# Optimization experiments

Measured on AMD Instinct MI355X. Metric: run time of the kernel, lower is better.

The kernel has to match this reference:

```python
import jax, jax.numpy as jnp
import numpy as np

N_BINS = 15


def setup_inputs() -> dict:
    key = jax.random.key(0)
    k1, k2 = jax.random.split(key)
    N, C = 2000000, 64
    probabilities = jax.random.uniform(k1, (N, C), dtype=jnp.float32)
    labels = jax.random.randint(k2, (N,), 0, C, dtype=jnp.int64)
    return {"probabilities": probabilities, "labels": labels}


def reference(probabilities, labels):
    # confidences/predictions over class dim
    confidences = jnp.max(probabilities, axis=1)
    predictions = jnp.argmax(probabilities, axis=1)
    accuracies = (predictions == labels).astype(confidences.dtype)

    boundaries = jnp.linspace(0.0, 1.0, N_BINS + 1)
    # torch loop uses (lower, upper] bins; digitize(right=True) gives index i
    # s.t. boundaries[i-1] < x <= boundaries[i]. conf == 0 falls in no bin.
    bin_idx = jnp.clip(jnp.digitize(confidences, boundaries, right=True) - 1, 0, N_BINS - 1)
    valid = (confidences > 0).astype(confidences.dtype)

    sum_conf = jax.ops.segment_sum(confidences * valid, bin_idx, num_segments=N_BINS)
    sum_acc = jax.ops.segment_sum(accuracies * valid, bin_idx, num_segments=N_BINS)
    count = jax.ops.segment_sum(valid, bin_idx, num_segments=N_BINS)

    n = confidences.shape[0]
    prop_in_bin = count / n
    safe = jnp.maximum(count, 1.0)
    avg_conf = sum_conf / safe
    avg_acc = sum_acc / safe
    per_bin = jnp.where(count > 0, jnp.abs(avg_conf - avg_acc) * prop_in_bin, 0.0)
    ece = jnp.sum(per_bin)
    return ece.reshape(1)
```

## Files before the change

kernel.cpp:

```cpp
#include <hip/hip_runtime.h>
#include <hip/hip_bf16.h>

#define N_BINS 15
#define C_DIM 64


__global__ void ece_main(const float* __restrict__ probs,
                         const int* __restrict__ labels,
                         float* __restrict__ gbins, int N) {
    __shared__ float s_conf[N_BINS];
    __shared__ float s_acc[N_BINS];
    __shared__ float s_cnt[N_BINS];

    const int tid = threadIdx.x;
    if (tid < N_BINS) { s_conf[tid] = 0.f; s_acc[tid] = 0.f; s_cnt[tid] = 0.f; }
    __syncthreads();

    const int lane = tid & 63;
    const int wave = tid >> 6;
    const int sub  = lane >> 4;
    const int l16  = lane & 15;
    const int wavesPerBlock = blockDim.x >> 6;

    long long g      = (long long)blockIdx.x * wavesPerBlock + wave;
    const long long gstride = (long long)gridDim.x * wavesPerBlock;

    for (; g * 4 < (long long)N; g += gstride) {
        const long long row = g * 4 + sub;
        const bool rowvalid = row < (long long)N;

        float conf; int pred;
        if (rowvalid) {
            const float4 v = *(const float4*)(probs + row * C_DIM + l16 * 4);
            float m = v.x; int a = l16 * 4;
            if (v.y > m) { m = v.y; a = l16 * 4 + 1; }
            if (v.z > m) { m = v.z; a = l16 * 4 + 2; }
            if (v.w > m) { m = v.w; a = l16 * 4 + 3; }
            conf = m; pred = a;
        } else {
            conf = -1.f; pred = 0;
        }

        #pragma unroll
        for (int off = 1; off < 16; off <<= 1) {
            float om = __shfl_xor(conf, off, 64);
            int   oa = __shfl_xor(pred, off, 64);
            if (om > conf || (om == conf && oa < pred)) { conf = om; pred = oa; }
        }

        if (l16 == 0 && rowvalid) {
            const int lab = labels[row];
            const float acc = (pred == lab) ? 1.f : 0.f;
            if (conf > 0.f) {
                int bin = (int)ceilf(conf * 15.f) - 1;
                bin = min(max(bin, 0), N_BINS - 1);
                atomicAdd(&s_conf[bin], conf);
                atomicAdd(&s_acc[bin], acc);
                atomicAdd(&s_cnt[bin], 1.f);
            }
        }
    }

    __syncthreads();
    if (tid < N_BINS) {
        atomicAdd(&gbins[tid],              s_conf[tid]);
        atomicAdd(&gbins[N_BINS + tid],     s_acc[tid]);
        atomicAdd(&gbins[2 * N_BINS + tid], s_cnt[tid]);
    }
}

__global__ void ece_final(const float* __restrict__ gbins,
                          float* __restrict__ out, int N) {
    if (threadIdx.x == 0 && blockIdx.x == 0) {
        float ece = 0.f;
        const float invN = 1.f / (float)N;
        for (int b = 0; b < N_BINS; b++) {
            const float sc = gbins[b];
            const float sa = gbins[N_BINS + b];
            const float cn = gbins[2 * N_BINS + b];
            if (cn > 0.f) {
                const float avg_conf = sc / cn;
                const float avg_acc  = sa / cn;
                ece += fabsf(avg_conf - avg_acc) * (cn * invN);
            }
        }
        out[0] = ece;
    }
}

extern "C" void kernel_launch(void* const* d_in, const int* in_sizes, int n_in,
                              void* d_out, int out_size, void* d_ws, size_t ws_size,
                              hipStream_t stream) {
    const float* probs  = (const float*)d_in[0];
    const int*   labels = (const int*)d_in[1];
    float* gbins = (float*)d_ws;
    float* out   = (float*)d_out;

    const int N = in_sizes[1];

    hipMemsetAsync(d_ws, 0, 3 * N_BINS * sizeof(float), stream);

    const int threads = 256;
    const int blocks  = 2048;
    ece_main<<<blocks, threads, 0, stream>>>(probs, labels, gbins, N);
    ece_final<<<1, 64, 0, stream>>>(gbins, out, N);
}
```

Baseline: 703.2 us.

## Process one row per thread and accumulate hot bins in registers

Each thread now owns a whole 64-float row, loading it as 16 float4s and running a serial argmax, which replaces the 16-lane cooperative load and the shuffle reduction. Bins 13 and 14, where the max of 64 uniform values almost always lands, are summed in per-thread registers and reduced with a wave shuffle, so shared-memory atomics are only needed for the rare low bins. The aim is to cut the shuffle and atomic contention overhead. The cost is uncoalesced per-thread row loads with a 256-byte stride and higher register pressure, which may reduce memory efficiency.

```diff
diff --git a/kernel.cpp b/kernel.cpp
--- a/kernel.cpp
+++ b/kernel.cpp
@@ -5,68 +5,69 @@
 #define C_DIM 64
 
 
-__global__ void ece_main(const float* __restrict__ probs,
-                         const int* __restrict__ labels,
-                         float* __restrict__ gbins, int N) {
-    __shared__ float s_conf[N_BINS];
-    __shared__ float s_acc[N_BINS];
-    __shared__ float s_cnt[N_BINS];
-
+__global__ __launch_bounds__(256) void ece_main(const float* __restrict__ probs,
+                                                const int* __restrict__ labels,
+                                                float* __restrict__ gbins, int N) {
+    __shared__ float s_bins[3 * N_BINS];
     const int tid = threadIdx.x;
-    if (tid < N_BINS) { s_conf[tid] = 0.f; s_acc[tid] = 0.f; s_cnt[tid] = 0.f; }
+    if (tid < 3 * N_BINS) s_bins[tid] = 0.f;
     __syncthreads();
 
-    const int lane = tid & 63;
-    const int wave = tid >> 6;
-    const int sub  = lane >> 4;
-    const int l16  = lane & 15;
-    const int wavesPerBlock = blockDim.x >> 6;
+    float c14 = 0.f, a14 = 0.f, n14 = 0.f;
+    float c13 = 0.f, a13 = 0.f, n13 = 0.f;
 
-    long long g      = (long long)blockIdx.x * wavesPerBlock + wave;
-    const long long gstride = (long long)gridDim.x * wavesPerBlock;
+    const int stride = gridDim.x * blockDim.x;
+    for (int row = blockIdx.x * blockDim.x + tid; row < N; row += stride) {
+        const int lab = labels[row];
+        const float4* p4 = (const float4*)(probs + (size_t)row * C_DIM);
 
-    for (; g * 4 < (long long)N; g += gstride) {
-        const long long row = g * 4 + sub;
-        const bool rowvalid = row < (long long)N;
+        float4 v[16];
+        #pragma unroll
+        for (int j = 0; j < 16; j++) v[j] = p4[j];
 
-        float conf; int pred;
-        if (rowvalid) {
-            const float4 v = *(const float4*)(probs + row * C_DIM + l16 * 4);
-            float m = v.x; int a = l16 * 4;
-            if (v.y > m) { m = v.y; a = l16 * 4 + 1; }
-            if (v.z > m) { m = v.z; a = l16 * 4 + 2; }
-            if (v.w > m) { m = v.w; a = l16 * 4 + 3; }
-            conf = m; pred = a;
-        } else {
-            conf = -1.f; pred = 0;
+        float best = v[0].x; int idx = 0;
+        #pragma unroll
+        for (int j = 0; j < 16; j++) {
+            if (v[j].x > best) { best = v[j].x; idx = 4 * j + 0; }
+            if (v[j].y > best) { best = v[j].y; idx = 4 * j + 1; }
+            if (v[j].z > best) { best = v[j].z; idx = 4 * j + 2; }
+            if (v[j].w > best) { best = v[j].w; idx = 4 * j + 3; }
         }
 
-        #pragma unroll
-        for (int off = 1; off < 16; off <<= 1) {
-            float om = __shfl_xor(conf, off, 64);
-            int   oa = __shfl_xor(pred, off, 64);
-            if (om > conf || (om == conf && oa < pred)) { conf = om; pred = oa; }
-        }
-
-        if (l16 == 0 && rowvalid) {
-            const int lab = labels[row];
-            const float acc = (pred == lab) ? 1.f : 0.f;
-            if (conf > 0.f) {
-                int bin = (int)ceilf(conf * 15.f) - 1;
-                bin = min(max(bin, 0), N_BINS - 1);
-                atomicAdd(&s_conf[bin], conf);
-                atomicAdd(&s_acc[bin], acc);
-                atomicAdd(&s_cnt[bin], 1.f);
+        const float conf = best;
+        const float acc = (idx == lab) ? 1.f : 0.f;
+        if (conf > 0.f) {
+            int bin = (int)ceilf(conf * 15.f) - 1;
+            bin = min(max(bin, 0), N_BINS - 1);
+            if (bin == 14)      { c14 += conf; a14 += acc; n14 += 1.f; }
+            else if (bin == 13) { c13 += conf; a13 += acc; n13 += 1.f; }
+            else {
+                atomicAdd(&s_bins[bin],             conf);
+                atomicAdd(&s_bins[N_BINS + bin],    acc);
+                atomicAdd(&s_bins[2 * N_BINS + bin], 1.f);
             }
         }
     }
 
+    #pragma unroll
+    for (int off = 32; off > 0; off >>= 1) {
+        c14 += __shfl_xor(c14, off, 64);
+        a14 += __shfl_xor(a14, off, 64);
+        n14 += __shfl_xor(n14, off, 64);
+        c13 += __shfl_xor(c13, off, 64);
+        a13 += __shfl_xor(a13, off, 64);
+        n13 += __shfl_xor(n13, off, 64);
+    }
+    if ((tid & 63) == 0) {
+        atomicAdd(&s_bins[14],              c14);
+        atomicAdd(&s_bins[N_BINS + 14],     a14);
+        atomicAdd(&s_bins[2 * N_BINS + 14], n14);
+        atomicAdd(&s_bins[13],              c13);
+        atomicAdd(&s_bins[N_BINS + 13],     a13);
+        atomicAdd(&s_bins[2 * N_BINS + 13], n13);
+    }
     __syncthreads();
-    if (tid < N_BINS) {
-        atomicAdd(&gbins[tid],              s_conf[tid]);
-        atomicAdd(&gbins[N_BINS + tid],     s_acc[tid]);
-        atomicAdd(&gbins[2 * N_BINS + tid], s_cnt[tid]);
-    }
+    if (tid < 3 * N_BINS) atomicAdd(&gbins[tid], s_bins[tid]);
 }
 
 __global__ void ece_final(const float* __restrict__ gbins,
```

Result: faster. 667.0 us (-5.1%).
